# Kernel tuning notes

Hardware: AMD Instinct MI355X
Metric: run time of the kernel (lower is better)

The kernel has to match this reference:

```python
import jax, jax.numpy as jnp
import numpy as np

K_PATCHES = 25
GRID_SIDE = 20            # sqrt(10000 // 25)
G = GRID_SIDE * GRID_SIDE # 400 points per patch
LATENT = 1024
DIMS = [LATENT + 2, 1024, 512, 256, 128, 3]  # per-layer in/out channels
BATCH = 16


def setup_inputs() -> dict:
    key = jax.random.key(0)
    ks = jax.random.split(key, 11)
    x = jax.random.normal(ks[0], (BATCH, LATENT), dtype=jnp.float32)
    params = {}
    # PyTorch Conv1d default init: U(-1/sqrt(fan_in), 1/sqrt(fan_in)); one weight set per patch.
    for i in range(5):
        fan_in = DIMS[i]
        bound = 1.0 / np.sqrt(fan_in)
        params[f"W{i+1}"] = jax.random.uniform(
            ks[1 + 2 * i], (K_PATCHES, DIMS[i], DIMS[i + 1]), jnp.float32, -bound, bound)
        params[f"b{i+1}"] = jax.random.uniform(
            ks[2 + 2 * i], (K_PATCHES, DIMS[i + 1]), jnp.float32, -bound, bound)
    return {"x": x, **params}


def reference(x, W1, b1, W2, b2, W3, b3, W4, b4, W5, b5):
    B = x.shape[0]
    # Deterministic UV grid (random_grid=False): same 20x20 grid for every patch.
    g = jnp.linspace(0.0, 1.0, GRID_SIDE)
    X, Y = jnp.meshgrid(g, g, indexing='xy')
    grid = jnp.stack([X, Y], axis=-1).reshape(-1, 2)  # (G, 2)
    # Build per-patch features: latent broadcast to every point + 2 uv coords.
    lat = jnp.broadcast_to(x[:, None, None, :], (B, K_PATCHES, G, LATENT))
    uv = jnp.broadcast_to(grid[None, None], (B, K_PATCHES, G, 2))
    h = jnp.concatenate([lat, uv], axis=-1)  # (B, P, G, 1026)
    # 1x1 Conv1d == per-point linear; batched over patches via grouped einsum.
    for W, b in ((W1, b1), (W2, b2), (W3, b3), (W4, b4)):
        h = jax.nn.relu(jnp.einsum('bpgi,pio->bpgo', h, W) + b[None, :, None, :])
    out = jnp.tanh(jnp.einsum('bpgi,pio->bpgo', h, W5) + b5[None, :, None, :])
    return out  # (B, P, G, 3) == torch stack(dim=1).permute(0,1,3,2)
```

## Files before the change

kernel.cpp:

```cpp
#include <hip/hip_runtime.h>
#include <math.h>

#define K_PATCHES 25
#define GRID_SIDE 20
#define G_PTS     400
#define LATENT    1024
#define BATCH     16

typedef _Float16 f16x8 __attribute__((ext_vector_type(8)));
typedef _Float16 f16x4 __attribute__((ext_vector_type(4)));
typedef float    f32x4 __attribute__((ext_vector_type(4)));

#define BASE_OFF 0
#define WT2_OFF  1638400
#define WT3_OFF  27852800
#define WT4_OFF  34406400

__global__ __launch_bounds__(128)
void base_kernel(const float* __restrict__ x,
                 const float* __restrict__ W1,
                 const float* __restrict__ b1,
                 float* __restrict__ base) {
    __shared__ float xs[BATCH][LATENT];
    const int p  = blockIdx.x >> 3;
    const int oc = blockIdx.x & 7;
    const int o  = oc * 128 + threadIdx.x;

    for (int idx = threadIdx.x; idx < BATCH * LATENT / 4; idx += 128)
        ((float4*)xs)[idx] = ((const float4*)x)[idx];
    __syncthreads();

    float acc[BATCH];
#pragma unroll
    for (int b = 0; b < BATCH; ++b) acc[b] = 0.0f;

    const float* Wp = W1 + (size_t)p * 1026 * 1024 + o;
    for (int k = 0; k < LATENT; k += 4) {
        const float w0 = Wp[(size_t)(k + 0) * 1024];
        const float w1 = Wp[(size_t)(k + 1) * 1024];
        const float w2 = Wp[(size_t)(k + 2) * 1024];
        const float w3 = Wp[(size_t)(k + 3) * 1024];
#pragma unroll
        for (int b = 0; b < BATCH; ++b) {
            const float4 xv = *(const float4*)&xs[b][k];
            acc[b] = fmaf(xv.w, w3, fmaf(xv.z, w2, fmaf(xv.y, w1, fmaf(xv.x, w0, acc[b]))));
        }
    }

    const float bias = b1[p * 1024 + o];
    for (int b = 0; b < BATCH; ++b)
        base[(size_t)(b * K_PATCHES + p) * 1024 + o] = acc[b] + bias;
}

__global__ __launch_bounds__(256)
void conv_tr_kernel(const float* __restrict__ W, _Float16* __restrict__ Wt,
                    int K, int N) {
    __shared__ float tile[64][65];
    const int tpp = (K / 64) * (N / 64);
    const int p   = blockIdx.x / tpp;
    const int rem = blockIdx.x % tpp;
    const int kt  = rem / (N / 64);
    const int nt  = rem % (N / 64);
    const int tr  = threadIdx.x >> 6;
    const int tc  = threadIdx.x & 63;

    const float* Wp = W + ((size_t)p * K + kt * 64) * N + nt * 64;
#pragma unroll
    for (int i = 0; i < 64; i += 4)
        tile[i + tr][tc] = Wp[(size_t)(i + tr) * N + tc];
    __syncthreads();

    _Float16* Wtp = Wt + ((size_t)p * N + nt * 64) * K + kt * 64;
#pragma unroll
    for (int i = 0; i < 64; i += 4)
        Wtp[(size_t)(i + tr) * K + tc] = (_Float16)tile[tc][i + tr];
}

__global__ __launch_bounds__(512)
void fused_mfma(const float* __restrict__ base,
                const float* __restrict__ W1,
                const _Float16* __restrict__ Wt2, const float* __restrict__ b2,
                const _Float16* __restrict__ Wt3, const float* __restrict__ b3,
                const _Float16* __restrict__ Wt4, const float* __restrict__ b4,
                const float* __restrict__ W5, const float* __restrict__ b5,
                float* __restrict__ out) {
    __shared__ __align__(16) unsigned char LDS[155648];
    constexpr int OFF_SB = 0;
    constexpr int OFF_WU = 8192;
    constexpr int OFF_WV = 12288;
    constexpr int OFF_H1 = 16384;
    constexpr int OFF_B2 = 24576;
    constexpr int OFF_H2 = 90112;
    constexpr int OFF_B3 = 0;
    constexpr int OFF_H3 = 32768;
    constexpr int OFF_B4 = 65536;
    constexpr int OFF_H4 = 81920;

    const int bid = blockIdx.x;
    const int xcd = bid & 7;
    const int ii  = bid >> 3;
    const int ord = (xcd < 4) ? xcd * 313 + ii : 4 * 313 + (xcd - 4) * 312 + ii;
    const int p     = ord / 100;
    const int rbase = (ord % 100) * 64;

    const int t    = threadIdx.x;
    const int lane = t & 63;
    const int w    = t >> 6;
    const int l16  = lane & 15;
    const int lq   = lane >> 4;

    float* sb0  = (float*)(LDS + OFF_SB);
    float* sb1  = sb0 + 1024;
    float* swuf = (float*)(LDS + OFF_WU);
    float* swvf = (float*)(LDS + OFF_WV);

    const int b0  = rbase / 400;
    const int b1i = (rbase + 63) / 400;
    {
        const float* base0 = base + (size_t)(b0 * K_PATCHES + p) * 1024;
        const float* base1 = base + (size_t)(b1i * K_PATCHES + p) * 1024;
        const float* wup   = W1 + (size_t)p * 1026 * 1024 + (size_t)1024 * 1024;
        if (t < 256) ((float4*)sb0)[t] = ((const float4*)base0)[t];
        else         ((float4*)sb1)[t - 256] = ((const float4*)base1)[t - 256];
        if (t < 256) ((float4*)swuf)[t] = ((const float4*)wup)[t];
        else         ((float4*)swvf)[t - 256] = ((const float4*)(wup + 1024))[t - 256];
    }
    __syncthreads();

    const int hm = t >> 3;
    const int hq = t & 7;
    const int rr = rbase + hm;
    const float* sbm = (rr < (b0 + 1) * 400) ? sb0 : sb1;
    const int g  = rr % 400;
    const float um = (float)(g % GRID_SIDE) * (1.0f / 19.0f);
    const float vm = (float)(g / GRID_SIDE) * (1.0f / 19.0f);
    const unsigned hwoff = (unsigned)(hm * 64 + (((hq >> 1) ^ (hm & 3)) << 4) + ((hq & 1) << 3));

    auto produce = [&](int kc, unsigned char* dst) {
        const float4 bv = *(const float4*)&sbm[kc + hq * 4];
        const float4 uu = *(const float4*)&swuf[kc + hq * 4];
        const float4 vv = *(const float4*)&swvf[kc + hq * 4];
        f16x4 hv;
        hv[0] = (_Float16)fmaxf(fmaf(vm, vv.x, fmaf(um, uu.x, bv.x)), 0.0f);
        hv[1] = (_Float16)fmaxf(fmaf(vm, vv.y, fmaf(um, uu.y, bv.y)), 0.0f);
        hv[2] = (_Float16)fmaxf(fmaf(vm, vv.z, fmaf(um, uu.z, bv.z)), 0.0f);
        hv[3] = (_Float16)fmaxf(fmaf(vm, vv.w, fmaf(um, uu.w, bv.w)), 0.0f);
        *(f16x4*)(dst + hwoff) = hv;
    };

    const _Float16* Wt2p = Wt2 + (size_t)p * 512 * 1024;
    f32x4 acc2[4][4];
    {
        const float* b2p = b2 + p * 512;
#pragma unroll
        for (int nf = 0; nf < 4; ++nf) {
            const float bias = b2p[w * 64 + nf * 16 + l16];
            f32x4 bv = {bias, bias, bias, bias};
#pragma unroll
            for (int mf = 0; mf < 4; ++mf) acc2[mf][nf] = bv;
        }
    }

    produce(0, LDS + OFF_H1);
    {
        f16x8 st[4];
#pragma unroll
        for (int j = 0; j < 4; ++j) {
            const int n = (t >> 2) + 128 * j;
            st[j] = *(const f16x8*)&Wt2p[(size_t)n * 1024 + (t & 3) * 8];
        }
        unsigned char* nb = LDS + OFF_B2;
#pragma unroll
        for (int j = 0; j < 4; ++j) {
            const int n = (t >> 2) + 128 * j;
            *(f16x8*)(nb + n * 64 + (((t & 3) ^ (n & 3)) << 4)) = st[j];
        }
    }
    __syncthreads();

#pragma unroll 1
    for (int c = 0; c < 32; ++c) {
        unsigned char* h1b = LDS + OFF_H1 + (c & 1) * 4096;
        unsigned char* b2b = LDS + OFF_B2 + (c & 1) * 32768;
        f16x8 st[4];
        const int kc1 = (c + 1) * 32;
        if (c < 31) {
#pragma unroll
            for (int j = 0; j < 4; ++j) {
                const int n = (t >> 2) + 128 * j;
                st[j] = *(const f16x8*)&Wt2p[(size_t)n * 1024 + kc1 + (t & 3) * 8];
            }
            produce(kc1, LDS + OFF_H1 + ((c + 1) & 1) * 4096);
        }
        f16x8 a[4], bfr[4];
#pragma unroll
        for (int mf = 0; mf < 4; ++mf) {
            const int r = mf * 16 + l16;
            a[mf] = *(const f16x8*)(h1b + r * 64 + ((lq ^ (r & 3)) << 4));
        }
#pragma unroll
        for (int nf = 0; nf < 4; ++nf) {
            const int n = w * 64 + nf * 16 + l16;
            bfr[nf] = *(const f16x8*)(b2b + n * 64 + ((lq ^ (n & 3)) << 4));
        }
        __builtin_amdgcn_s_setprio(1);
#pragma unroll
        for (int mf = 0; mf < 4; ++mf)
#pragma unroll
            for (int nf = 0; nf < 4; ++nf)
                acc2[mf][nf] = __builtin_amdgcn_mfma_f32_16x16x32_f16(a[mf], bfr[nf], acc2[mf][nf], 0, 0, 0);
        __builtin_amdgcn_s_setprio(0);
        if (c < 31) {
            unsigned char* nb = LDS + OFF_B2 + ((c + 1) & 1) * 32768;
#pragma unroll
            for (int j = 0; j < 4; ++j) {
                const int n = (t >> 2) + 128 * j;
                *(f16x8*)(nb + n * 64 + (((t & 3) ^ (n & 3)) << 4)) = st[j];
            }
        }
        __syncthreads();
    }

#pragma unroll
    for (int mf = 0; mf < 4; ++mf)
#pragma unroll
        for (int nf = 0; nf < 4; ++nf)
#pragma unroll
            for (int r = 0; r < 4; ++r) {
                const int row = mf * 16 + lq * 4 + r;
                const int col = w * 64 + nf * 16 + l16;
                const float v = fmaxf(acc2[mf][nf][r], 0.0f);
                *(_Float16*)(LDS + OFF_H2 + ((row * 1024 + col * 2) ^ ((row & 7) << 4))) = (_Float16)v;
            }

    const _Float16* Wt3p = Wt3 + (size_t)p * 256 * 512;
    f32x4 acc3[4][2];
    {
        const float* b3p = b3 + p * 256;
#pragma unroll
        for (int nf = 0; nf < 2; ++nf) {
            const float bias = b3p[w * 32 + nf * 16 + l16];
            f32x4 bv = {bias, bias, bias, bias};
#pragma unroll
            for (int mf = 0; mf < 4; ++mf) acc3[mf][nf] = bv;
        }
    }
    {
        f16x8 st[2];
#pragma unroll
        for (int j = 0; j < 2; ++j) {
            const int n = (t >> 2) + 128 * j;
            st[j] = *(const f16x8*)&Wt3p[(size_t)n * 512 + (t & 3) * 8];
        }
        unsigned char* nb = LDS + OFF_B3;
#pragma unroll
        for (int j = 0; j < 2; ++j) {
            const int n = (t >> 2) + 128 * j;
            *(f16x8*)(nb + n * 64 + (((t & 3) ^ (n & 3)) << 4)) = st[j];
        }
    }
    __syncthreads();

#pragma unroll 1
    for (int c = 0; c < 16; ++c) {
        unsigned char* b3b = LDS + OFF_B3 + (c & 1) * 16384;
        const int kc = c * 32;
        f16x8 st[2];
        if (c < 15) {
            const int kc1 = kc + 32;
#pragma unroll
            for (int j = 0; j < 2; ++j) {
                const int n = (t >> 2) + 128 * j;
                st[j] = *(const f16x8*)&Wt3p[(size_t)n * 512 + kc1 + (t & 3) * 8];
            }
        }
        f16x8 a[4], bfr[2];
#pragma unroll
        for (int mf = 0; mf < 4; ++mf) {
            const int r = mf * 16 + l16;
            a[mf] = *(const f16x8*)(LDS + OFF_H2 + ((r * 1024 + (kc + lq * 8) * 2) ^ ((r & 7) << 4)));
        }
#pragma unroll
        for (int nf = 0; nf < 2; ++nf) {
            const int n = w * 32 + nf * 16 + l16;
            bfr[nf] = *(const f16x8*)(b3b + n * 64 + ((lq ^ (n & 3)) << 4));
        }
        __builtin_amdgcn_s_setprio(1);
#pragma unroll
        for (int mf = 0; mf < 4; ++mf)
#pragma unroll
            for (int nf = 0; nf < 2; ++nf)
                acc3[mf][nf] = __builtin_amdgcn_mfma_f32_16x16x32_f16(a[mf], bfr[nf], acc3[mf][nf], 0, 0, 0);
        __builtin_amdgcn_s_setprio(0);
        if (c < 15) {
            unsigned char* nb = LDS + OFF_B3 + ((c + 1) & 1) * 16384;
#pragma unroll
            for (int j = 0; j < 2; ++j) {
                const int n = (t >> 2) + 128 * j;
                *(f16x8*)(nb + n * 64 + (((t & 3) ^ (n & 3)) << 4)) = st[j];
            }
        }
        __syncthreads();
    }

#pragma unroll
    for (int mf = 0; mf < 4; ++mf)
#pragma unroll
        for (int nf = 0; nf < 2; ++nf)
#pragma unroll
            for (int r = 0; r < 4; ++r) {
                const int row = mf * 16 + lq * 4 + r;
                const int col = w * 32 + nf * 16 + l16;
                const float v = fmaxf(acc3[mf][nf][r], 0.0f);
                *(_Float16*)(LDS + OFF_H3 + ((row * 512 + col * 2) ^ ((row & 7) << 4))) = (_Float16)v;
            }

    const _Float16* Wt4p = Wt4 + (size_t)p * 128 * 256;
    f32x4 acc4[4];
    {
        const float* b4p = b4 + p * 128;
        const float bias = b4p[w * 16 + l16];
        f32x4 bv = {bias, bias, bias, bias};
#pragma unroll
        for (int mf = 0; mf < 4; ++mf) acc4[mf] = bv;
    }
    {
        const int n = t >> 2;
        f16x8 st0 = *(const f16x8*)&Wt4p[(size_t)n * 256 + (t & 3) * 8];
        *(f16x8*)(LDS + OFF_B4 + n * 64 + (((t & 3) ^ (n & 3)) << 4)) = st0;
    }
    __syncthreads();

#pragma unroll 1
    for (int c = 0; c < 8; ++c) {
        unsigned char* b4b = LDS + OFF_B4 + (c & 1) * 8192;
        const int kc = c * 32;
        f16x8 st0;
        if (c < 7) {
            const int n = t >> 2;
            st0 = *(const f16x8*)&Wt4p[(size_t)n * 256 + kc + 32 + (t & 3) * 8];
        }
        f16x8 a[4], bfr;
#pragma unroll
        for (int mf = 0; mf < 4; ++mf) {
            const int r = mf * 16 + l16;
            a[mf] = *(const f16x8*)(LDS + OFF_H3 + ((r * 512 + (kc + lq * 8) * 2) ^ ((r & 7) << 4)));
        }
        {
            const int n = w * 16 + l16;
            bfr = *(const f16x8*)(b4b + n * 64 + ((lq ^ (n & 3)) << 4));
        }
        __builtin_amdgcn_s_setprio(1);
#pragma unroll
        for (int mf = 0; mf < 4; ++mf)
            acc4[mf] = __builtin_amdgcn_mfma_f32_16x16x32_f16(a[mf], bfr, acc4[mf], 0, 0, 0);
        __builtin_amdgcn_s_setprio(0);
        if (c < 7) {
            unsigned char* nb = LDS + OFF_B4 + ((c + 1) & 1) * 8192;
            const int n = t >> 2;
            *(f16x8*)(nb + n * 64 + (((t & 3) ^ (n & 3)) << 4)) = st0;
        }
        __syncthreads();
    }

#pragma unroll
    for (int mf = 0; mf < 4; ++mf)
#pragma unroll
        for (int r = 0; r < 4; ++r) {
            const int row = mf * 16 + lq * 4 + r;
            const int col = w * 16 + l16;
            const float v = fmaxf(acc4[mf][r], 0.0f);
            *(_Float16*)(LDS + OFF_H4 + ((row * 256 + col * 2) ^ ((row & 7) << 4))) = (_Float16)v;
        }
    __syncthreads();

    if (t < 192) {
        const int m = t / 3;
        const int c = t % 3;
        const float* W5p = W5 + p * 128 * 3;
        float acc = b5[p * 3 + c];
#pragma unroll 4
        for (int k = 0; k < 128; ++k) {
            const _Float16 hv = *(const _Float16*)(LDS + OFF_H4 + ((m * 256 + k * 2) ^ ((m & 7) << 4)));
            acc = fmaf((float)hv, W5p[k * 3 + c], acc);
        }
        const int r  = rbase + m;
        const int bb = r / 400;
        const int gg = r % 400;
        out[((size_t)(bb * K_PATCHES + p) * G_PTS + gg) * 3 + c] = tanhf(acc);
    }
}

extern "C" void kernel_launch(void* const* d_in, const int* in_sizes, int n_in,
                              void* d_out, int out_size, void* d_ws, size_t ws_size,
                              hipStream_t stream) {
    const float* x  = (const float*)d_in[0];
    const float* W1 = (const float*)d_in[1];
    const float* b1 = (const float*)d_in[2];
    const float* W2 = (const float*)d_in[3];
    const float* b2 = (const float*)d_in[4];
    const float* W3 = (const float*)d_in[5];
    const float* b3 = (const float*)d_in[6];
    const float* W4 = (const float*)d_in[7];
    const float* b4 = (const float*)d_in[8];
    const float* W5 = (const float*)d_in[9];
    const float* b5 = (const float*)d_in[10];
    float* out = (float*)d_out;

    float*     base = (float*)((char*)d_ws + BASE_OFF);
    _Float16*  Wt2  = (_Float16*)((char*)d_ws + WT2_OFF);
    _Float16*  Wt3  = (_Float16*)((char*)d_ws + WT3_OFF);
    _Float16*  Wt4  = (_Float16*)((char*)d_ws + WT4_OFF);

    base_kernel<<<K_PATCHES * 8, 128, 0, stream>>>(x, W1, b1, base);

    conv_tr_kernel<<<K_PATCHES * (1024 / 64) * (512 / 64), 256, 0, stream>>>(W2, Wt2, 1024, 512);
    conv_tr_kernel<<<K_PATCHES * (512 / 64) * (256 / 64),  256, 0, stream>>>(W3, Wt3, 512, 256);
    conv_tr_kernel<<<K_PATCHES * (256 / 64) * (128 / 64),  256, 0, stream>>>(W4, Wt4, 256, 128);

    fused_mfma<<<K_PATCHES * 100, 512, 0, stream>>>(
        base, W1, Wt2, b2, Wt3, b3, Wt4, b4, W5, b5, out);
}
```

Measured before the change: 517.1 us.

## Load MFMA weight fragments directly from global into registers, drop LDS staging

```diff
diff --git a/kernel.cpp b/kernel.cpp
--- a/kernel.cpp
+++ b/kernel.cpp
@@ -84,17 +84,14 @@
                 const _Float16* __restrict__ Wt4, const float* __restrict__ b4,
                 const float* __restrict__ W5, const float* __restrict__ b5,
                 float* __restrict__ out) {
-    __shared__ __align__(16) unsigned char LDS[155648];
+    __shared__ __align__(16) unsigned char LDS[139264];
     constexpr int OFF_SB = 0;
     constexpr int OFF_WU = 8192;
     constexpr int OFF_WV = 12288;
     constexpr int OFF_H1 = 16384;
-    constexpr int OFF_B2 = 24576;
-    constexpr int OFF_H2 = 90112;
-    constexpr int OFF_B3 = 0;
-    constexpr int OFF_H3 = 32768;
-    constexpr int OFF_B4 = 65536;
-    constexpr int OFF_H4 = 81920;
+    constexpr int OFF_H2 = 24576;
+    constexpr int OFF_H3 = 90112;
+    constexpr int OFF_H4 = 122880;
 
     const int bid = blockIdx.x;
     const int xcd = bid & 7;
@@ -127,28 +124,30 @@
     }
     __syncthreads();
 
-    const int hm = t >> 3;
-    const int hq = t & 7;
-    const int rr = rbase + hm;
-    const float* sbm = (rr < (b0 + 1) * 400) ? sb0 : sb1;
-    const int g  = rr % 400;
-    const float um = (float)(g % GRID_SIDE) * (1.0f / 19.0f);
-    const float vm = (float)(g / GRID_SIDE) * (1.0f / 19.0f);
-    const unsigned hwoff = (unsigned)(hm * 64 + (((hq >> 1) ^ (hm & 3)) << 4) + ((hq & 1) << 3));
-
-    auto produce = [&](int kc, unsigned char* dst) {
-        const float4 bv = *(const float4*)&sbm[kc + hq * 4];
-        const float4 uu = *(const float4*)&swuf[kc + hq * 4];
-        const float4 vv = *(const float4*)&swvf[kc + hq * 4];
+    const int pko   = t >> 7;
+    const int pr    = (t >> 1) & 63;
+    const int phalf = t & 1;
+    const float* sbm2 = (rbase + pr < (b0 + 1) * 400) ? sb0 : sb1;
+    const int pg  = (rbase + pr) % 400;
+    const float pu = (float)(pg % GRID_SIDE) * (1.0f / 19.0f);
+    const float pv = (float)(pg / GRID_SIDE) * (1.0f / 19.0f);
+    const unsigned pwoff = (unsigned)((pko * 64 + pr) * 16 + phalf * 8);
+
+    auto produce2 = [&](int kc, unsigned char* dst) {
+        const int k = kc + pko * 8 + phalf * 4;
+        const float4 bv = *(const float4*)&sbm2[k];
+        const float4 uu = *(const float4*)&swuf[k];
+        const float4 vv = *(const float4*)&swvf[k];
         f16x4 hv;
-        hv[0] = (_Float16)fmaxf(fmaf(vm, vv.x, fmaf(um, uu.x, bv.x)), 0.0f);
-        hv[1] = (_Float16)fmaxf(fmaf(vm, vv.y, fmaf(um, uu.y, bv.y)), 0.0f);
-        hv[2] = (_Float16)fmaxf(fmaf(vm, vv.z, fmaf(um, uu.z, bv.z)), 0.0f);
-        hv[3] = (_Float16)fmaxf(fmaf(vm, vv.w, fmaf(um, uu.w, bv.w)), 0.0f);
-        *(f16x4*)(dst + hwoff) = hv;
+        hv[0] = (_Float16)fmaxf(fmaf(pv, vv.x, fmaf(pu, uu.x, bv.x)), 0.0f);
+        hv[1] = (_Float16)fmaxf(fmaf(pv, vv.y, fmaf(pu, uu.y, bv.y)), 0.0f);
+        hv[2] = (_Float16)fmaxf(fmaf(pv, vv.z, fmaf(pu, uu.z, bv.z)), 0.0f);
+        hv[3] = (_Float16)fmaxf(fmaf(pv, vv.w, fmaf(pu, uu.w, bv.w)), 0.0f);
+        *(f16x4*)(dst + pwoff) = hv;
     };
 
     const _Float16* Wt2p = Wt2 + (size_t)p * 512 * 1024;
+    const _Float16* b2base = Wt2p + (size_t)(w * 64 + l16) * 1024 + lq * 8;
     f32x4 acc2[4][4];
     {
         const float* b2p = b2 + p * 512;
@@ -161,64 +160,40 @@
         }
     }
 
-    produce(0, LDS + OFF_H1);
-    {
-        f16x8 st[4];
-#pragma unroll
-        for (int j = 0; j < 4; ++j) {
-            const int n = (t >> 2) + 128 * j;
-            st[j] = *(const f16x8*)&Wt2p[(size_t)n * 1024 + (t & 3) * 8];
-        }
-        unsigned char* nb = LDS + OFF_B2;
-#pragma unroll
-        for (int j = 0; j < 4; ++j) {
-            const int n = (t >> 2) + 128 * j;
-            *(f16x8*)(nb + n * 64 + (((t & 3) ^ (n & 3)) << 4)) = st[j];
-        }
-    }
-    __syncthreads();
+    f16x8 bA[4], bB[4];
+    produce2(0, LDS + OFF_H1);
+#pragma unroll
+    for (int nf = 0; nf < 4; ++nf)
+        bA[nf] = *(const f16x8*)(b2base + (size_t)nf * 16384);
+    __syncthreads();
+
+    auto l2step = [&](int c, f16x8 (&bc)[4], f16x8 (&bn)[4]) {
+        const unsigned char* h1b = LDS + OFF_H1 + (c & 1) * 4096;
+        if (c < 31) {
+            const int kc1 = (c + 1) * 32;
+#pragma unroll
+            for (int nf = 0; nf < 4; ++nf)
+                bn[nf] = *(const f16x8*)(b2base + (size_t)nf * 16384 + kc1);
+            produce2(kc1, LDS + OFF_H1 + ((c + 1) & 1) * 4096);
+        }
+        f16x8 a[4];
+#pragma unroll
+        for (int mf = 0; mf < 4; ++mf)
+            a[mf] = *(const f16x8*)(h1b + (lq * 64 + mf * 16 + l16) * 16);
+        __builtin_amdgcn_s_setprio(1);
+#pragma unroll
+        for (int mf = 0; mf < 4; ++mf)
+#pragma unroll
+            for (int nf = 0; nf < 4; ++nf)
+                acc2[mf][nf] = __builtin_amdgcn_mfma_f32_16x16x32_f16(a[mf], bc[nf], acc2[mf][nf], 0, 0, 0);
+        __builtin_amdgcn_s_setprio(0);
+        __syncthreads();
+    };
 
 #pragma unroll 1
-    for (int c = 0; c < 32; ++c) {
-        unsigned char* h1b = LDS + OFF_H1 + (c & 1) * 4096;
-        unsigned char* b2b = LDS + OFF_B2 + (c & 1) * 32768;
-        f16x8 st[4];
-        const int kc1 = (c + 1) * 32;
-        if (c < 31) {
-#pragma unroll
-            for (int j = 0; j < 4; ++j) {
-                const int n = (t >> 2) + 128 * j;
-                st[j] = *(const f16x8*)&Wt2p[(size_t)n * 1024 + kc1 + (t & 3) * 8];
-            }
-            produce(kc1, LDS + OFF_H1 + ((c + 1) & 1) * 4096);
-        }
-        f16x8 a[4], bfr[4];
-#pragma unroll
-        for (int mf = 0; mf < 4; ++mf) {
-            const int r = mf * 16 + l16;
-            a[mf] = *(const f16x8*)(h1b + r * 64 + ((lq ^ (r & 3)) << 4));
-        }
-#pragma unroll
-        for (int nf = 0; nf < 4; ++nf) {
-            const int n = w * 64 + nf * 16 + l16;
-            bfr[nf] = *(const f16x8*)(b2b + n * 64 + ((lq ^ (n & 3)) << 4));
-        }
-        __builtin_amdgcn_s_setprio(1);
-#pragma unroll
-        for (int mf = 0; mf < 4; ++mf)
-#pragma unroll
-            for (int nf = 0; nf < 4; ++nf)
-                acc2[mf][nf] = __builtin_amdgcn_mfma_f32_16x16x32_f16(a[mf], bfr[nf], acc2[mf][nf], 0, 0, 0);
-        __builtin_amdgcn_s_setprio(0);
-        if (c < 31) {
-            unsigned char* nb = LDS + OFF_B2 + ((c + 1) & 1) * 32768;
-#pragma unroll
-            for (int j = 0; j < 4; ++j) {
-                const int n = (t >> 2) + 128 * j;
-                *(f16x8*)(nb + n * 64 + (((t & 3) ^ (n & 3)) << 4)) = st[j];
-            }
-        }
-        __syncthreads();
+    for (int c = 0; c < 32; c += 2) {
+        l2step(c,     bA, bB);
+        l2step(c + 1, bB, bA);
     }
 
 #pragma unroll
@@ -230,10 +205,12 @@
                 const int row = mf * 16 + lq * 4 + r;
                 const int col = w * 64 + nf * 16 + l16;
                 const float v = fmaxf(acc2[mf][nf][r], 0.0f);
-                *(_Float16*)(LDS + OFF_H2 + ((row * 1024 + col * 2) ^ ((row & 7) << 4))) = (_Float16)v;
+                *(_Float16*)(LDS + OFF_H2 + ((col >> 3) * 64 + row) * 16 + (col & 7) * 2) = (_Float16)v;
             }
+    __syncthreads();
 
     const _Float16* Wt3p = Wt3 + (size_t)p * 256 * 512;
+    const _Float16* b3base = Wt3p + (size_t)(w * 32 + l16) * 512 + lq * 8;
     f32x4 acc3[4][2];
     {
         const float* b3p = b3 + p * 256;
@@ -245,62 +222,35 @@
             for (int mf = 0; mf < 4; ++mf) acc3[mf][nf] = bv;
         }
     }
-    {
-        f16x8 st[2];
-#pragma unroll
-        for (int j = 0; j < 2; ++j) {
-            const int n = (t >> 2) + 128 * j;
-            st[j] = *(const f16x8*)&Wt3p[(size_t)n * 512 + (t & 3) * 8];
-        }
-        unsigned char* nb = LDS + OFF_B3;
-#pragma unroll
-        for (int j = 0; j < 2; ++j) {
-            const int n = (t >> 2) + 128 * j;
-            *(f16x8*)(nb + n * 64 + (((t & 3) ^ (n & 3)) << 4)) = st[j];
-        }
-    }
-    __syncthreads();
+    f16x8 cA[2], cB[2];
+#pragma unroll
+    for (int nf = 0; nf < 2; ++nf)
+        cA[nf] = *(const f16x8*)(b3base + (size_t)nf * 8192);
+
+    auto l3step = [&](int c, f16x8 (&bc)[2], f16x8 (&bn)[2]) {
+        if (c < 15) {
+            const int kc1 = (c + 1) * 32;
+#pragma unroll
+            for (int nf = 0; nf < 2; ++nf)
+                bn[nf] = *(const f16x8*)(b3base + (size_t)nf * 8192 + kc1);
+        }
+        f16x8 a[4];
+#pragma unroll
+        for (int mf = 0; mf < 4; ++mf)
+            a[mf] = *(const f16x8*)(LDS + OFF_H2 + ((c * 4 + lq) * 64 + mf * 16 + l16) * 16);
+        __builtin_amdgcn_s_setprio(1);
+#pragma unroll
+        for (int mf = 0; mf < 4; ++mf)
+#pragma unroll
+            for (int nf = 0; nf < 2; ++nf)
+                acc3[mf][nf] = __builtin_amdgcn_mfma_f32_16x16x32_f16(a[mf], bc[nf], acc3[mf][nf], 0, 0, 0);
+        __builtin_amdgcn_s_setprio(0);
+    };
 
 #pragma unroll 1
-    for (int c = 0; c < 16; ++c) {
-        unsigned char* b3b = LDS + OFF_B3 + (c & 1) * 16384;
-        const int kc = c * 32;
-        f16x8 st[2];
-        if (c < 15) {
-            const int kc1 = kc + 32;
-#pragma unroll
-            for (int j = 0; j < 2; ++j) {
-                const int n = (t >> 2) + 128 * j;
-                st[j] = *(const f16x8*)&Wt3p[(size_t)n * 512 + kc1 + (t & 3) * 8];
-            }
-        }
-        f16x8 a[4], bfr[2];
-#pragma unroll
-        for (int mf = 0; mf < 4; ++mf) {
-            const int r = mf * 16 + l16;
-            a[mf] = *(const f16x8*)(LDS + OFF_H2 + ((r * 1024 + (kc + lq * 8) * 2) ^ ((r & 7) << 4)));
-        }
-#pragma unroll
-        for (int nf = 0; nf < 2; ++nf) {
-            const int n = w * 32 + nf * 16 + l16;
-            bfr[nf] = *(const f16x8*)(b3b + n * 64 + ((lq ^ (n & 3)) << 4));
-        }
-        __builtin_amdgcn_s_setprio(1);
-#pragma unroll
-        for (int mf = 0; mf < 4; ++mf)
-#pragma unroll
-            for (int nf = 0; nf < 2; ++nf)
-                acc3[mf][nf] = __builtin_amdgcn_mfma_f32_16x16x32_f16(a[mf], bfr[nf], acc3[mf][nf], 0, 0, 0);
-        __builtin_amdgcn_s_setprio(0);
-        if (c < 15) {
-            unsigned char* nb = LDS + OFF_B3 + ((c + 1) & 1) * 16384;
-#pragma unroll
-            for (int j = 0; j < 2; ++j) {
-                const int n = (t >> 2) + 128 * j;
-                *(f16x8*)(nb + n * 64 + (((t & 3) ^ (n & 3)) << 4)) = st[j];
-            }
-        }
-        __syncthreads();
+    for (int c = 0; c < 16; c += 2) {
+        l3step(c,     cA, cB);
+        l3step(c + 1, cB, cA);
     }
 
 #pragma unroll
@@ -312,10 +262,12 @@
                 const int row = mf * 16 + lq * 4 + r;
                 const int col = w * 32 + nf * 16 + l16;
                 const float v = fmaxf(acc3[mf][nf][r], 0.0f);
-                *(_Float16*)(LDS + OFF_H3 + ((row * 512 + col * 2) ^ ((row & 7) << 4))) = (_Float16)v;
+                *(_Float16*)(LDS + OFF_H3 + ((col >> 3) * 64 + row) * 16 + (col & 7) * 2) = (_Float16)v;
             }
+    __syncthreads();
 
     const _Float16* Wt4p = Wt4 + (size_t)p * 128 * 256;
+    const _Float16* b4base = Wt4p + (size_t)(w * 16 + l16) * 256 + lq * 8;
     f32x4 acc4[4];
     {
         const float* b4p = b4 + p * 128;
@@ -324,43 +276,27 @@
 #pragma unroll
         for (int mf = 0; mf < 4; ++mf) acc4[mf] = bv;
     }
-    {
-        const int n = t >> 2;
-        f16x8 st0 = *(const f16x8*)&Wt4p[(size_t)n * 256 + (t & 3) * 8];
-        *(f16x8*)(LDS + OFF_B4 + n * 64 + (((t & 3) ^ (n & 3)) << 4)) = st0;
-    }
-    __syncthreads();
+    f16x8 dA, dB;
+    dA = *(const f16x8*)(b4base);
+
+    auto l4step = [&](int c, f16x8& bc, f16x8& bn) {
+        if (c < 7)
+            bn = *(const f16x8*)(b4base + (c + 1) * 32);
+        f16x8 a[4];
+#pragma unroll
+        for (int mf = 0; mf < 4; ++mf)
+            a[mf] = *(const f16x8*)(LDS + OFF_H3 + ((c * 4 + lq) * 64 + mf * 16 + l16) * 16);
+        __builtin_amdgcn_s_setprio(1);
+#pragma unroll
+        for (int mf = 0; mf < 4; ++mf)
+            acc4[mf] = __builtin_amdgcn_mfma_f32_16x16x32_f16(a[mf], bc, acc4[mf], 0, 0, 0);
+        __builtin_amdgcn_s_setprio(0);
+    };
 
 #pragma unroll 1
-    for (int c = 0; c < 8; ++c) {
-        unsigned char* b4b = LDS + OFF_B4 + (c & 1) * 8192;
-        const int kc = c * 32;
-        f16x8 st0;
-        if (c < 7) {
-            const int n = t >> 2;
-            st0 = *(const f16x8*)&Wt4p[(size_t)n * 256 + kc + 32 + (t & 3) * 8];
-        }
-        f16x8 a[4], bfr;
-#pragma unroll
-        for (int mf = 0; mf < 4; ++mf) {
-            const int r = mf * 16 + l16;
-            a[mf] = *(const f16x8*)(LDS + OFF_H3 + ((r * 512 + (kc + lq * 8) * 2) ^ ((r & 7) << 4)));
-        }
-        {
-            const int n = w * 16 + l16;
-            bfr = *(const f16x8*)(b4b + n * 64 + ((lq ^ (n & 3)) << 4));
-        }
-        __builtin_amdgcn_s_setprio(1);
-#pragma unroll
-        for (int mf = 0; mf < 4; ++mf)
-            acc4[mf] = __builtin_amdgcn_mfma_f32_16x16x32_f16(a[mf], bfr, acc4[mf], 0, 0, 0);
-        __builtin_amdgcn_s_setprio(0);
-        if (c < 7) {
-            unsigned char* nb = LDS + OFF_B4 + ((c + 1) & 1) * 8192;
-            const int n = t >> 2;
-            *(f16x8*)(nb + n * 64 + (((t & 3) ^ (n & 3)) << 4)) = st0;
-        }
-        __syncthreads();
+    for (int c = 0; c < 8; c += 2) {
+        l4step(c,     dA, dB);
+        l4step(c + 1, dB, dA);
     }
 
 #pragma unroll
@@ -370,7 +306,7 @@
             const int row = mf * 16 + lq * 4 + r;
             const int col = w * 16 + l16;
             const float v = fmaxf(acc4[mf][r], 0.0f);
-            *(_Float16*)(LDS + OFF_H4 + ((row * 256 + col * 2) ^ ((row & 7) << 4))) = (_Float16)v;
+            *(_Float16*)(LDS + OFF_H4 + ((col >> 3) * 64 + row) * 16 + (col & 7) * 2) = (_Float16)v;
         }
     __syncthreads();
 
@@ -381,7 +317,7 @@
         float acc = b5[p * 3 + c];
 #pragma unroll 4
         for (int k = 0; k < 128; ++k) {
-            const _Float16 hv = *(const _Float16*)(LDS + OFF_H4 + ((m * 256 + k * 2) ^ ((m & 7) << 4)));
+            const _Float16 hv = *(const _Float16*)(LDS + OFF_H4 + ((k >> 3) * 64 + m) * 16 + (k & 7) * 2);
             acc = fmaf((float)hv, W5p[k * 3 + c], acc);
         }
         const int r  = rbase + m;
```

Measured after the change: 594.5 us. 1.15x slower.
